# Optimization experiments

Hardware: AMD Instinct MI355X
Metric: run time of the kernel (lower is better)

The kernel has to match this reference:

```python
import jax, jax.numpy as jnp
import numpy as np

D_MODEL = 512
WINDOW = 128
N_HEADS = 8


def setup_inputs() -> dict:
    key = jax.random.key(0)
    k1, k2, k3, k4, k5 = jax.random.split(key, 5)
    B, S, D = 8, 4096, D_MODEL
    scale = 1.0 / np.sqrt(D)
    return {
        "x": jax.random.normal(k1, (B, S, D), dtype=jnp.float32),
        "in_proj_w": jax.random.normal(k2, (3 * D, D), dtype=jnp.float32) * scale,
        "in_proj_b": jax.random.normal(k3, (3 * D,), dtype=jnp.float32) * 0.02,
        "out_proj_w": jax.random.normal(k4, (D, D), dtype=jnp.float32) * scale,
        "out_proj_b": jax.random.normal(k5, (D,), dtype=jnp.float32) * 0.02,
    }


def reference(x, in_proj_w, in_proj_b, out_proj_w, out_proj_b):
    # Non-overlapping sliding-window MHA with shared weights per window.
    B, S, D = x.shape
    W = WINDOW
    H = N_HEADS
    hd = D // H
    nw = S // W  # S chosen divisible by window size

    xw = x.reshape(B, nw, W, D)
    # Fused QKV projection (torch in_proj_weight layout: [3D, D], y = x @ W^T + b)
    qkv = jnp.einsum("bnwd,ed->bnwe", xw, in_proj_w) + in_proj_b  # [B,nw,W,3D]
    q, k, v = jnp.split(qkv, 3, axis=-1)

    def to_heads(t):
        return t.reshape(B, nw, W, H, hd)

    q = to_heads(q) * (1.0 / np.sqrt(hd))
    k = to_heads(k)
    v = to_heads(v)

    # Block-diagonal attention: scores only within each window [B,nw,H,W,W]
    scores = jnp.einsum("bnqhd,bnkhd->bnhqk", q, k)
    attn = jax.nn.softmax(scores, axis=-1)
    ctx = jnp.einsum("bnhqk,bnkhd->bnqhd", attn, v)  # [B,nw,W,H,hd]
    ctx = ctx.reshape(B, S, D)

    out = jnp.einsum("bsd,ed->bse", ctx, out_proj_w) + out_proj_b
    return out
```

## Files before the change

### kernel.cpp

```cpp
#include <hip/hip_runtime.h>


typedef __bf16 bf16x8 __attribute__((ext_vector_type(8)));
typedef float  f32x4  __attribute__((ext_vector_type(4)));

#define MFMA16(a, b, c) __builtin_amdgcn_mfma_f32_16x16x32_bf16((a), (b), (c), 0, 0, 0)

#define VMCNT_(n) asm volatile("s_waitcnt vmcnt(" #n ")" ::: "memory")
#define VMCNT(n) VMCNT_(n)
#define LGKM0() asm volatile("s_waitcnt lgkmcnt(0)" ::: "memory")

__device__ __forceinline__ void gload_lds16(const __bf16* g, void* l) {
    __builtin_amdgcn_global_load_lds(
        (const __attribute__((address_space(1))) unsigned int*)g,
        (__attribute__((address_space(3))) unsigned int*)l, 16, 0, 0);
}

__device__ __forceinline__ void cvt8(const float* __restrict__ s,
                                     __bf16* __restrict__ d, long i) {
    const float4* s4 = reinterpret_cast<const float4*>(s);
    float4 a = s4[2 * i], b = s4[2 * i + 1];
    bf16x8 v;
    v[0] = (__bf16)a.x; v[1] = (__bf16)a.y; v[2] = (__bf16)a.z; v[3] = (__bf16)a.w;
    v[4] = (__bf16)b.x; v[5] = (__bf16)b.y; v[6] = (__bf16)b.z; v[7] = (__bf16)b.w;
    *reinterpret_cast<bf16x8*>(d + 8 * i) = v;
}

__global__ void convert_k(const float* __restrict__ x,
                          const float* __restrict__ w_in,
                          const float* __restrict__ w_out,
                          __bf16* __restrict__ x_bf,
                          __bf16* __restrict__ w_in_bf,
                          __bf16* __restrict__ w_out_bf)
{
    long i0 = (long)blockIdx.x * blockDim.x + threadIdx.x;
    long stride = (long)gridDim.x * blockDim.x;
    for (long i = i0; i < 16777216 / 8; i += stride) cvt8(x, x_bf, i);
    for (long i = i0; i < 786432 / 8;   i += stride) cvt8(w_in, w_in_bf, i);
    for (long i = i0; i < 262144 / 8;   i += stride) cvt8(w_out, w_out_bf, i);
}

template<int EPI, int NN>
__global__ __launch_bounds__(512, 2)
void gemm256(const __bf16* __restrict__ A,
             const __bf16* __restrict__ Bw,
             const float* __restrict__ bias,
             void* __restrict__ Cq,
             __bf16* __restrict__ vT)
{
    __shared__ __align__(16) char smem[131072];

    const int nwg = gridDim.x;
    const int chunk = nwg >> 3;
    const int bid = blockIdx.x;
    const int wg = (bid & 7) * chunk + (bid >> 3);
    const int nidx = wg % NN;
    const int midx = wg / NN;
    const long mbase = (long)midx * 256;
    const int colbase = nidx * 256;

    const int tid = threadIdx.x;
    const int w = tid >> 6, lane = tid & 63;
    const int lrow = lane & 15, hi = lane >> 4;
    const int quad = lane >> 4, sl = lane & 15;
    const int wm = w >> 2, wn = w & 3;

    const int l8 = lane >> 3;
    const int slotp = (lane & 7) ^ l8;
    const __bf16* stA = A  + (mbase + 8 * w + l8) * 512 + slotp * 8;
    const __bf16* stB = Bw + ((long)colbase + 8 * w + l8) * 512 + slotp * 8;
    const int ldsw = w * 1024;

    auto stage8 = [&](int tt) {
        char* As = smem + (tt & 1) * 32768;
        char* Bs = smem + 65536 + (tt & 1) * 32768;
        const int ko = tt * 64;
        gload_lds16(stA + ko,             As + ldsw);
        gload_lds16(stA + 64 * 512 + ko,  As + 8192 + ldsw);
        gload_lds16(stA + 128 * 512 + ko, As + 16384 + ldsw);
        gload_lds16(stA + 192 * 512 + ko, As + 24576 + ldsw);
        gload_lds16(stB + ko,             Bs + ldsw);
        gload_lds16(stB + 64 * 512 + ko,  Bs + 8192 + ldsw);
        gload_lds16(stB + 128 * 512 + ko, Bs + 16384 + ldsw);
        gload_lds16(stB + 192 * 512 + ko, Bs + 24576 + ldsw);
    };

    f32x4 acc[8][4];
    #pragma unroll
    for (int rt = 0; rt < 8; ++rt)
        #pragma unroll
        for (int ct = 0; ct < 4; ++ct) acc[rt][ct] = (f32x4){0.f, 0.f, 0.f, 0.f};

    bf16x8 af[4], bfr[4];

#define PHASE(T, KK, RT0, LB)                                                     \
    {                                                                             \
        const char* As = smem + ((T) & 1) * 32768;                                \
        const char* Bs = smem + 65536 + ((T) & 1) * 32768;                        \
        const int ko = ((KK) * 64 + hi * 16) ^ ((lrow & 7) << 4);                 \
        if (LB) {                                                                 \
            _Pragma("unroll")                                                     \
            for (int ct = 0; ct < 4; ++ct)                                        \
                bfr[ct] = *reinterpret_cast<const bf16x8*>(                       \
                    Bs + (64 * wn + 16 * ct + lrow) * 128 + ko);                  \
        }                                                                         \
        _Pragma("unroll")                                                         \
        for (int i = 0; i < 4; ++i)                                               \
            af[i] = *reinterpret_cast<const bf16x8*>(                             \
                As + (128 * wm + 16 * ((RT0) + i) + lrow) * 128 + ko);            \
        __builtin_amdgcn_s_setprio(1);                                            \
        _Pragma("unroll")                                                         \
        for (int i = 0; i < 4; ++i)                                               \
            _Pragma("unroll")                                                     \
            for (int ct = 0; ct < 4; ++ct)                                        \
                acc[(RT0) + i][ct] = MFMA16(af[i], bfr[ct], acc[(RT0) + i][ct]);  \
        __builtin_amdgcn_s_setprio(0);                                            \
    }

    stage8(0); stage8(1);
    VMCNT(8);
    __builtin_amdgcn_s_barrier();

    #pragma unroll 1
    for (int t = 0; t < 8; ++t) {
        if (t) {
            VMCNT(0);
            __builtin_amdgcn_s_barrier();
            if (t < 7) stage8(t + 1);
        }
        PHASE(t, 0, 0, 1);
        __builtin_amdgcn_s_barrier();
        PHASE(t, 0, 4, 0);
        __builtin_amdgcn_s_barrier();
        PHASE(t, 1, 0, 1);
        __builtin_amdgcn_s_barrier();
        PHASE(t, 1, 4, 0);
    }
#undef PHASE
    __builtin_amdgcn_s_barrier();

    const int colg0 = colbase + 64 * wn + lrow;
    if (EPI == 0) {
        if (colbase < 1024) {
            const float scale = (colbase < 512) ? 0.125f : 1.0f;
            __bf16* qk = (__bf16*)Cq;
            #pragma unroll
            for (int ct = 0; ct < 4; ++ct) {
                float b = bias[colg0 + 16 * ct];
                int col2 = (64 * wn + 16 * ct + lrow) * 2;
                #pragma unroll
                for (int rt = 0; rt < 8; ++rt)
                    #pragma unroll
                    for (int r = 0; r < 4; ++r) {
                        int row = 128 * wm + 16 * rt + 4 * hi + r;
                        *reinterpret_cast<__bf16*>(
                            smem + row * 512 + (col2 ^ ((row & 31) << 4))) =
                            (__bf16)((acc[rt][ct][r] + b) * scale);
                    }
            }
            LGKM0();
            __builtin_amdgcn_s_barrier();
            #pragma unroll
            for (int i = 0; i < 8; ++i) {
                int row = 32 * w + 4 * i + quad;
                #pragma unroll
                for (int h2 = 0; h2 < 2; ++h2) {
                    int slot = (16 * h2 + sl) ^ (row & 31);
                    bf16x8 v = *reinterpret_cast<const bf16x8*>(smem + row * 512 + slot * 16);
                    *reinterpret_cast<bf16x8*>(
                        qk + (mbase + row) * 1024 + colbase + h2 * 128 + sl * 8) = v;
                }
            }
        } else {
            #pragma unroll
            for (int ct = 0; ct < 4; ++ct) {
                float b = bias[colg0 + 16 * ct];
                int e = 64 * wn + 16 * ct + lrow;
                #pragma unroll
                for (int rt = 0; rt < 8; ++rt)
                    #pragma unroll
                    for (int r = 0; r < 4; ++r) {
                        int tok = 128 * wm + 16 * rt + 4 * hi + r;
                        *reinterpret_cast<__bf16*>(
                            smem + e * 512 + ((tok * 2) ^ ((e & 31) << 4))) =
                            (__bf16)(acc[rt][ct][r] + b);
                    }
            }
            LGKM0();
            __builtin_amdgcn_s_barrier();
            #pragma unroll
            for (int i = 0; i < 8; ++i) {
                int e = 32 * w + 4 * i + quad;
                #pragma unroll
                for (int h2 = 0; h2 < 2; ++h2) {
                    int slot = (16 * h2 + sl) ^ (e & 31);
                    bf16x8 v = *reinterpret_cast<const bf16x8*>(smem + e * 512 + slot * 16);
                    *reinterpret_cast<bf16x8*>(
                        vT + (long)(2 * midx + h2) * 65536 +
                        (colbase - 1024 + e) * 128 + sl * 8) = v;
                }
            }
        }
    } else {
        float* outp = (float*)Cq;
        float bb[4];
        #pragma unroll
        for (int ct = 0; ct < 4; ++ct) bb[ct] = bias[colg0 + 16 * ct];
        #pragma unroll 1
        for (int half = 0; half < 2; ++half) {
            if (wm == half) {
                #pragma unroll
                for (int ct = 0; ct < 4; ++ct) {
                    int c4 = (64 * wn + 16 * ct + lrow) * 4;
                    #pragma unroll
                    for (int rt = 0; rt < 8; ++rt)
                        #pragma unroll
                        for (int r = 0; r < 4; ++r) {
                            int row = 16 * rt + 4 * hi + r;
                            *reinterpret_cast<float*>(
                                smem + row * 1024 + (c4 ^ ((row & 63) << 4))) =
                                acc[rt][ct][r] + bb[ct];
                        }
                }
            }
            LGKM0();
            __builtin_amdgcn_s_barrier();
            #pragma unroll
            for (int i = 0; i < 4; ++i) {
                int row = 16 * w + 4 * i + quad;
                #pragma unroll
                for (int h2 = 0; h2 < 4; ++h2) {
                    int slot = (16 * h2 + sl) ^ (row & 63);
                    f32x4 v = *reinterpret_cast<const f32x4*>(smem + row * 1024 + slot * 16);
                    *reinterpret_cast<f32x4*>(
                        outp + (mbase + 128 * half + row) * 512 + colbase + h2 * 64 + sl * 4) = v;
                }
            }
            __builtin_amdgcn_s_barrier();
        }
    }
}

__global__ __launch_bounds__(256)
void swa_attn(const __bf16* __restrict__ qk,
              const __bf16* __restrict__ vT,
              __bf16* __restrict__ ctx)
{
    __shared__ __bf16 p_lds[4][32][136];

    const int bid = blockIdx.x;
    const int win = bid >> 3, h = bid & 7;
    const int tid = threadIdx.x;
    const int w = tid >> 6, lane = tid & 63;
    const int lrow = lane & 15, hi = lane >> 4;
    const long tokb = (long)win * 128;

    bf16x8 qa[2][2];
    #pragma unroll
    for (int rt = 0; rt < 2; ++rt)
        #pragma unroll
        for (int ks = 0; ks < 2; ++ks)
            qa[rt][ks] = *reinterpret_cast<const bf16x8*>(
                qk + (tokb + 32 * w + 16 * rt + lrow) * 1024 + h * 64 + ks * 32 + hi * 8);

    f32x4 s[2][8];
    #pragma unroll
    for (int rt = 0; rt < 2; ++rt)
        #pragma unroll
        for (int ct = 0; ct < 8; ++ct) s[rt][ct] = (f32x4){0.f, 0.f, 0.f, 0.f};
    #pragma unroll
    for (int ks = 0; ks < 2; ++ks) {
        #pragma unroll
        for (int ct = 0; ct < 8; ++ct) {
            bf16x8 kb = *reinterpret_cast<const bf16x8*>(
                qk + (tokb + 16 * ct + lrow) * 1024 + 512 + h * 64 + ks * 32 + hi * 8);
            s[0][ct] = MFMA16(qa[0][ks], kb, s[0][ct]);
            s[1][ct] = MFMA16(qa[1][ks], kb, s[1][ct]);
        }
    }

    float inv[2][4];
    #pragma unroll
    for (int rt = 0; rt < 2; ++rt) {
        #pragma unroll
        for (int r = 0; r < 4; ++r) {
            float m = s[rt][0][r];
            #pragma unroll
            for (int ct = 1; ct < 8; ++ct) m = fmaxf(m, s[rt][ct][r]);
            m = fmaxf(m, __shfl_xor(m, 1));
            m = fmaxf(m, __shfl_xor(m, 2));
            m = fmaxf(m, __shfl_xor(m, 4));
            m = fmaxf(m, __shfl_xor(m, 8));
            float sum = 0.f;
            #pragma unroll
            for (int ct = 0; ct < 8; ++ct) {
                float e = __expf(s[rt][ct][r] - m);
                sum += e;
                p_lds[w][16 * rt + 4 * hi + r][16 * ct + lrow] = (__bf16)e;
            }
            sum += __shfl_xor(sum, 1);
            sum += __shfl_xor(sum, 2);
            sum += __shfl_xor(sum, 4);
            sum += __shfl_xor(sum, 8);
            inv[rt][r] = 1.f / sum;
        }
    }

    f32x4 o[2][4];
    #pragma unroll
    for (int rt = 0; rt < 2; ++rt)
        #pragma unroll
        for (int ct = 0; ct < 4; ++ct) o[rt][ct] = (f32x4){0.f, 0.f, 0.f, 0.f};
    const __bf16* vb = vT + ((long)win * 8 + h) * 64 * 128;
    #pragma unroll
    for (int kt = 0; kt < 4; ++kt) {
        bf16x8 pa0 = *reinterpret_cast<const bf16x8*>(&p_lds[w][lrow][32 * kt + 8 * hi]);
        bf16x8 pa1 = *reinterpret_cast<const bf16x8*>(&p_lds[w][16 + lrow][32 * kt + 8 * hi]);
        #pragma unroll
        for (int ct = 0; ct < 4; ++ct) {
            bf16x8 vf = *reinterpret_cast<const bf16x8*>(
                vb + (16 * ct + lrow) * 128 + 32 * kt + 8 * hi);
            o[0][ct] = MFMA16(pa0, vf, o[0][ct]);
            o[1][ct] = MFMA16(pa1, vf, o[1][ct]);
        }
    }

    #pragma unroll
    for (int rt = 0; rt < 2; ++rt)
        #pragma unroll
        for (int ct = 0; ct < 4; ++ct)
            #pragma unroll
            for (int r = 0; r < 4; ++r) {
                long tok = tokb + 32 * w + 16 * rt + 4 * hi + r;
                ctx[tok * 512 + h * 64 + 16 * ct + lrow] =
                    (__bf16)(o[rt][ct][r] * inv[rt][r]);
            }
}

extern "C" void kernel_launch(void* const* d_in, const int* in_sizes, int n_in,
                              void* d_out, int out_size, void* d_ws, size_t ws_size,
                              hipStream_t stream)
{
    const float* x     = (const float*)d_in[0];
    const float* w_in  = (const float*)d_in[1];
    const float* b_in  = (const float*)d_in[2];
    const float* w_out = (const float*)d_in[3];
    const float* b_out = (const float*)d_in[4];

    char* ws = (char*)d_ws;
    __bf16* x_bf     = (__bf16*)(ws);
    __bf16* ctx      = (__bf16*)(ws);
    __bf16* vT       = (__bf16*)(ws + 33554432);
    __bf16* w_in_bf  = (__bf16*)(ws + 67108864);
    __bf16* w_out_bf = (__bf16*)(ws + 68681728);
    __bf16* qk       = (__bf16*)d_out;

    convert_k<<<2048, 256, 0, stream>>>(x, w_in, w_out, x_bf, w_in_bf, w_out_bf);
    gemm256<0, 6><<<768, 512, 0, stream>>>(x_bf, w_in_bf, b_in, (void*)qk, vT);
    swa_attn<<<2048, 256, 0, stream>>>(qk, vT, ctx);
    gemm256<1, 2><<<256, 512, 0, stream>>>(ctx, w_out_bf, b_out, d_out, nullptr);
}
```

Before: 177.2 us.

## Fuse QKV projection with windowed attention per window, simplify output GEMM epilogue

Replaces the separate QKV GEMM and attention kernels with one kernel where each block owns a 128-token window. It loops over heads, computes that head's Q/K/V slice of the projection into LDS, then does softmax attention in place. This avoids writing Q, K and V^T to global memory and reading them back. The cost is only 256 blocks, head-serial work with many barriers, and re-reading the x tile for every head. The output GEMM epilogue now writes scattered fp32 directly instead of staging through LDS for coalesced stores.

```diff
diff --git a/kernel.cpp b/kernel.cpp
--- a/kernel.cpp
+++ b/kernel.cpp
@@ -5,7 +5,6 @@
 typedef float  f32x4  __attribute__((ext_vector_type(4)));
 
 #define MFMA16(a, b, c) __builtin_amdgcn_mfma_f32_16x16x32_bf16((a), (b), (c), 0, 0, 0)
-
 #define VMCNT_(n) asm volatile("s_waitcnt vmcnt(" #n ")" ::: "memory")
 #define VMCNT(n) VMCNT_(n)
 #define LGKM0() asm volatile("s_waitcnt lgkmcnt(0)" ::: "memory")
@@ -40,13 +39,177 @@
     for (long i = i0; i < 262144 / 8;   i += stride) cvt8(w_out, w_out_bf, i);
 }
 
-template<int EPI, int NN>
 __global__ __launch_bounds__(512, 2)
-void gemm256(const __bf16* __restrict__ A,
-             const __bf16* __restrict__ Bw,
-             const float* __restrict__ bias,
-             void* __restrict__ Cq,
-             __bf16* __restrict__ vT)
+void swa_fused(const __bf16* __restrict__ x_bf,
+               const __bf16* __restrict__ w_in,
+               const float* __restrict__ b_in,
+               __bf16* __restrict__ ctx)
+{
+    __shared__ __align__(16) char smem[134144];
+    char* const ring = smem;
+    char* const q_l  = smem;
+    char* const k_l  = smem + 18432;
+    char* const vT_l = smem + 81920;
+    char* const p_l  = smem + 99328;
+
+    const int win = blockIdx.x;
+    const long tokb = (long)win * 128;
+    const int tid = threadIdx.x, w = tid >> 6, lane = tid & 63;
+    const int lrow = lane & 15, hi = lane >> 4;
+    const int rw = w >> 2, cw = w & 3;
+    const int l8 = lane >> 3;
+    const int slotp = (lane & 7) ^ l8;
+
+    const __bf16* Ax  = x_bf + (tokb + 8 * w + l8) * 512 + slotp * 8;
+    const __bf16* Bx0 = w_in + (long)(8 * w + l8) * 512 + slotp * 8;
+
+    auto stage = [&](int h, int t) {
+        char* buf = ring + (t & 1) * 40960;
+        const int ko = t * 64;
+        const __bf16* Bx = Bx0 + (long)h * 64 * 512;
+        gload_lds16(Ax + ko,                    buf + w * 1024);
+        gload_lds16(Ax + 64 * 512 + ko,         buf + 8192 + w * 1024);
+        gload_lds16(Bx + ko,                    buf + 16384 + w * 1024);
+        gload_lds16(Bx + (long)512 * 512 + ko,  buf + 24576 + w * 1024);
+        gload_lds16(Bx + (long)1024 * 512 + ko, buf + 32768 + w * 1024);
+    };
+
+    stage(0, 0);
+
+    #pragma unroll 1
+    for (int h = 0; h < 8; ++h) {
+        f32x4 acc[4][3];
+        #pragma unroll
+        for (int i = 0; i < 4; ++i)
+            #pragma unroll
+            for (int j = 0; j < 3; ++j) acc[i][j] = (f32x4){0.f, 0.f, 0.f, 0.f};
+
+        #pragma unroll 1
+        for (int t = 0; t < 8; ++t) {
+            VMCNT(0);
+            LGKM0();
+            __builtin_amdgcn_s_barrier();
+            if (t < 7) stage(h, t + 1);
+            const char* As = ring + (t & 1) * 40960;
+            const char* Bs = As + 16384;
+            #pragma unroll
+            for (int kk = 0; kk < 2; ++kk) {
+                const int ko = (kk * 64 + hi * 16) ^ ((lrow & 7) << 4);
+                bf16x8 af[4], bfr[3];
+                #pragma unroll
+                for (int i = 0; i < 4; ++i)
+                    af[i] = *reinterpret_cast<const bf16x8*>(
+                        As + (64 * rw + 16 * i + lrow) * 128 + ko);
+                #pragma unroll
+                for (int j = 0; j < 3; ++j)
+                    bfr[j] = *reinterpret_cast<const bf16x8*>(
+                        Bs + (48 * cw + 16 * j + lrow) * 128 + ko);
+                __builtin_amdgcn_s_setprio(1);
+                #pragma unroll
+                for (int i = 0; i < 4; ++i)
+                    #pragma unroll
+                    for (int j = 0; j < 3; ++j)
+                        acc[i][j] = MFMA16(af[i], bfr[j], acc[i][j]);
+                __builtin_amdgcn_s_setprio(0);
+            }
+        }
+        LGKM0();
+        __builtin_amdgcn_s_barrier();
+
+        #pragma unroll
+        for (int j = 0; j < 3; ++j) {
+            const int n = 48 * cw + 16 * j + lrow;
+            const int band = n >> 6, d = n & 63;
+            const float bb = b_in[band * 512 + h * 64 + d];
+            #pragma unroll
+            for (int i = 0; i < 4; ++i)
+                #pragma unroll
+                for (int r = 0; r < 4; ++r) {
+                    const int m = 64 * rw + 16 * i + 4 * hi + r;
+                    const float v = acc[i][j][r] + bb;
+                    if (band == 0)
+                        *reinterpret_cast<__bf16*>(q_l + m * 144 + d * 2) = (__bf16)(v * 0.125f);
+                    else if (band == 1)
+                        *reinterpret_cast<__bf16*>(k_l + m * 144 + d * 2) = (__bf16)v;
+                    else
+                        *reinterpret_cast<__bf16*>(vT_l + d * 272 + m * 2) = (__bf16)v;
+                }
+        }
+        LGKM0();
+        __builtin_amdgcn_s_barrier();
+
+        f32x4 s[8];
+        #pragma unroll
+        for (int ct = 0; ct < 8; ++ct) s[ct] = (f32x4){0.f, 0.f, 0.f, 0.f};
+        #pragma unroll
+        for (int kt = 0; kt < 2; ++kt) {
+            bf16x8 qa = *reinterpret_cast<const bf16x8*>(
+                q_l + (16 * w + lrow) * 144 + kt * 64 + hi * 16);
+            #pragma unroll
+            for (int ct = 0; ct < 8; ++ct) {
+                bf16x8 kb = *reinterpret_cast<const bf16x8*>(
+                    k_l + (16 * ct + lrow) * 144 + kt * 64 + hi * 16);
+                s[ct] = MFMA16(qa, kb, s[ct]);
+            }
+        }
+        LGKM0();
+        __builtin_amdgcn_s_barrier();
+        if (h < 7) stage(h + 1, 0);
+
+        float inv[4];
+        #pragma unroll
+        for (int r = 0; r < 4; ++r) {
+            float mx = s[0][r];
+            #pragma unroll
+            for (int ct = 1; ct < 8; ++ct) mx = fmaxf(mx, s[ct][r]);
+            mx = fmaxf(mx, __shfl_xor(mx, 1));
+            mx = fmaxf(mx, __shfl_xor(mx, 2));
+            mx = fmaxf(mx, __shfl_xor(mx, 4));
+            mx = fmaxf(mx, __shfl_xor(mx, 8));
+            float sum = 0.f;
+            #pragma unroll
+            for (int ct = 0; ct < 8; ++ct) {
+                float e = __expf(s[ct][r] - mx);
+                sum += e;
+                *reinterpret_cast<__bf16*>(
+                    p_l + w * 4352 + (4 * hi + r) * 272 + (16 * ct + lrow) * 2) = (__bf16)e;
+            }
+            sum += __shfl_xor(sum, 1);
+            sum += __shfl_xor(sum, 2);
+            sum += __shfl_xor(sum, 4);
+            sum += __shfl_xor(sum, 8);
+            inv[r] = 1.f / sum;
+        }
+
+        f32x4 o[4];
+        #pragma unroll
+        for (int ct = 0; ct < 4; ++ct) o[ct] = (f32x4){0.f, 0.f, 0.f, 0.f};
+        #pragma unroll
+        for (int kt = 0; kt < 4; ++kt) {
+            bf16x8 pa = *reinterpret_cast<const bf16x8*>(
+                p_l + w * 4352 + lrow * 272 + kt * 64 + hi * 16);
+            #pragma unroll
+            for (int ct = 0; ct < 4; ++ct) {
+                bf16x8 vf = *reinterpret_cast<const bf16x8*>(
+                    vT_l + (16 * ct + lrow) * 272 + kt * 64 + hi * 16);
+                o[ct] = MFMA16(pa, vf, o[ct]);
+            }
+        }
+        #pragma unroll
+        for (int ct = 0; ct < 4; ++ct)
+            #pragma unroll
+            for (int r = 0; r < 4; ++r) {
+                long tok = tokb + 16 * w + 4 * hi + r;
+                ctx[tok * 512 + h * 64 + 16 * ct + lrow] = (__bf16)(o[ct][r] * inv[r]);
+            }
+    }
+}
+
+__global__ __launch_bounds__(512, 2)
+void gemm_out(const __bf16* __restrict__ A,
+              const __bf16* __restrict__ Bw,
+              const float* __restrict__ bias,
+              float* __restrict__ out)
 {
     __shared__ __align__(16) char smem[131072];
 
@@ -54,15 +217,14 @@
     const int chunk = nwg >> 3;
     const int bid = blockIdx.x;
     const int wg = (bid & 7) * chunk + (bid >> 3);
-    const int nidx = wg % NN;
-    const int midx = wg / NN;
+    const int nidx = wg % 2;
+    const int midx = wg / 2;
     const long mbase = (long)midx * 256;
     const int colbase = nidx * 256;
 
     const int tid = threadIdx.x;
     const int w = tid >> 6, lane = tid & 63;
     const int lrow = lane & 15, hi = lane >> 4;
-    const int quad = lane >> 4, sl = lane & 15;
     const int wm = w >> 2, wn = w & 3;
 
     const int l8 = lane >> 3;
@@ -92,7 +254,6 @@
         for (int ct = 0; ct < 4; ++ct) acc[rt][ct] = (f32x4){0.f, 0.f, 0.f, 0.f};
 
     bf16x8 af[4], bfr[4];
-
 #define PHASE(T, KK, RT0, LB)                                                     \
     {                                                                             \
         const char* As = smem + ((T) & 1) * 32768;                                \
@@ -137,204 +298,19 @@
         PHASE(t, 1, 4, 0);
     }
 #undef PHASE
-    __builtin_amdgcn_s_barrier();
-
-    const int colg0 = colbase + 64 * wn + lrow;
-    if (EPI == 0) {
-        if (colbase < 1024) {
-            const float scale = (colbase < 512) ? 0.125f : 1.0f;
-            __bf16* qk = (__bf16*)Cq;
-            #pragma unroll
-            for (int ct = 0; ct < 4; ++ct) {
-                float b = bias[colg0 + 16 * ct];
-                int col2 = (64 * wn + 16 * ct + lrow) * 2;
-                #pragma unroll
-                for (int rt = 0; rt < 8; ++rt)
-                    #pragma unroll
-                    for (int r = 0; r < 4; ++r) {
-                        int row = 128 * wm + 16 * rt + 4 * hi + r;
-                        *reinterpret_cast<__bf16*>(
-                            smem + row * 512 + (col2 ^ ((row & 31) << 4))) =
-                            (__bf16)((acc[rt][ct][r] + b) * scale);
-                    }
-            }
-            LGKM0();
-            __builtin_amdgcn_s_barrier();
-            #pragma unroll
-            for (int i = 0; i < 8; ++i) {
-                int row = 32 * w + 4 * i + quad;
-                #pragma unroll
-                for (int h2 = 0; h2 < 2; ++h2) {
-                    int slot = (16 * h2 + sl) ^ (row & 31);
-                    bf16x8 v = *reinterpret_cast<const bf16x8*>(smem + row * 512 + slot * 16);
-                    *reinterpret_cast<bf16x8*>(
-                        qk + (mbase + row) * 1024 + colbase + h2 * 128 + sl * 8) = v;
-                }
-            }
-        } else {
-            #pragma unroll
-            for (int ct = 0; ct < 4; ++ct) {
-                float b = bias[colg0 + 16 * ct];
-                int e = 64 * wn + 16 * ct + lrow;
-                #pragma unroll
-                for (int rt = 0; rt < 8; ++rt)
-                    #pragma unroll
-                    for (int r = 0; r < 4; ++r) {
-                        int tok = 128 * wm + 16 * rt + 4 * hi + r;
-                        *reinterpret_cast<__bf16*>(
-                            smem + e * 512 + ((tok * 2) ^ ((e & 31) << 4))) =
-                            (__bf16)(acc[rt][ct][r] + b);
-                    }
-            }
-            LGKM0();
-            __builtin_amdgcn_s_barrier();
-            #pragma unroll
-            for (int i = 0; i < 8; ++i) {
-                int e = 32 * w + 4 * i + quad;
-                #pragma unroll
-                for (int h2 = 0; h2 < 2; ++h2) {
-                    int slot = (16 * h2 + sl) ^ (e & 31);
-                    bf16x8 v = *reinterpret_cast<const bf16x8*>(smem + e * 512 + slot * 16);
-                    *reinterpret_cast<bf16x8*>(
-                        vT + (long)(2 * midx + h2) * 65536 +
-                        (colbase - 1024 + e) * 128 + sl * 8) = v;
-                }
-            }
-        }
-    } else {
-        float* outp = (float*)Cq;
-        float bb[4];
-        #pragma unroll
-        for (int ct = 0; ct < 4; ++ct) bb[ct] = bias[colg0 + 16 * ct];
-        #pragma unroll 1
-        for (int half = 0; half < 2; ++half) {
-            if (wm == half) {
-                #pragma unroll
-                for (int ct = 0; ct < 4; ++ct) {
-                    int c4 = (64 * wn + 16 * ct + lrow) * 4;
-                    #pragma unroll
-                    for (int rt = 0; rt < 8; ++rt)
-                        #pragma unroll
-                        for (int r = 0; r < 4; ++r) {
-                            int row = 16 * rt + 4 * hi + r;
-                            *reinterpret_cast<float*>(
-                                smem + row * 1024 + (c4 ^ ((row & 63) << 4))) =
-                                acc[rt][ct][r] + bb[ct];
-                        }
-                }
-            }
-            LGKM0();
-            __builtin_amdgcn_s_barrier();
-            #pragma unroll
-            for (int i = 0; i < 4; ++i) {
-                int row = 16 * w + 4 * i + quad;
-                #pragma unroll
-                for (int h2 = 0; h2 < 4; ++h2) {
-                    int slot = (16 * h2 + sl) ^ (row & 63);
-                    f32x4 v = *reinterpret_cast<const f32x4*>(smem + row * 1024 + slot * 16);
-                    *reinterpret_cast<f32x4*>(
-                        outp + (mbase + 128 * half + row) * 512 + colbase + h2 * 64 + sl * 4) = v;
-                }
-            }
-            __builtin_amdgcn_s_barrier();
+
+    #pragma unroll
+    for (int ct = 0; ct < 4; ++ct) {
+        int colg = colbase + 64 * wn + 16 * ct + lrow;
+        float b = bias[colg];
+        #pragma unroll
+        for (int rt = 0; rt < 8; ++rt) {
+            long row = mbase + 128 * wm + 16 * rt + 4 * hi;
+            #pragma unroll
+            for (int r = 0; r < 4; ++r)
+                out[(row + r) * 512 + colg] = acc[rt][ct][r] + b;
         }
     }
-}
-
-__global__ __launch_bounds__(256)
-void swa_attn(const __bf16* __restrict__ qk,
-              const __bf16* __restrict__ vT,
-              __bf16* __restrict__ ctx)
-{
-    __shared__ __bf16 p_lds[4][32][136];
-
-    const int bid = blockIdx.x;
-    const int win = bid >> 3, h = bid & 7;
-    const int tid = threadIdx.x;
-    const int w = tid >> 6, lane = tid & 63;
-    const int lrow = lane & 15, hi = lane >> 4;
-    const long tokb = (long)win * 128;
-
-    bf16x8 qa[2][2];
-    #pragma unroll
-    for (int rt = 0; rt < 2; ++rt)
-        #pragma unroll
-        for (int ks = 0; ks < 2; ++ks)
-            qa[rt][ks] = *reinterpret_cast<const bf16x8*>(
-                qk + (tokb + 32 * w + 16 * rt + lrow) * 1024 + h * 64 + ks * 32 + hi * 8);
-
-    f32x4 s[2][8];
-    #pragma unroll
-    for (int rt = 0; rt < 2; ++rt)
-        #pragma unroll
-        for (int ct = 0; ct < 8; ++ct) s[rt][ct] = (f32x4){0.f, 0.f, 0.f, 0.f};
-    #pragma unroll
-    for (int ks = 0; ks < 2; ++ks) {
-        #pragma unroll
-        for (int ct = 0; ct < 8; ++ct) {
-            bf16x8 kb = *reinterpret_cast<const bf16x8*>(
-                qk + (tokb + 16 * ct + lrow) * 1024 + 512 + h * 64 + ks * 32 + hi * 8);
-            s[0][ct] = MFMA16(qa[0][ks], kb, s[0][ct]);
-            s[1][ct] = MFMA16(qa[1][ks], kb, s[1][ct]);
-        }
-    }
-
-    float inv[2][4];
-    #pragma unroll
-    for (int rt = 0; rt < 2; ++rt) {
-        #pragma unroll
-        for (int r = 0; r < 4; ++r) {
-            float m = s[rt][0][r];
-            #pragma unroll
-            for (int ct = 1; ct < 8; ++ct) m = fmaxf(m, s[rt][ct][r]);
-            m = fmaxf(m, __shfl_xor(m, 1));
-            m = fmaxf(m, __shfl_xor(m, 2));
-            m = fmaxf(m, __shfl_xor(m, 4));
-            m = fmaxf(m, __shfl_xor(m, 8));
-            float sum = 0.f;
-            #pragma unroll
-            for (int ct = 0; ct < 8; ++ct) {
-                float e = __expf(s[rt][ct][r] - m);
-                sum += e;
-                p_lds[w][16 * rt + 4 * hi + r][16 * ct + lrow] = (__bf16)e;
-            }
-            sum += __shfl_xor(sum, 1);
-            sum += __shfl_xor(sum, 2);
-            sum += __shfl_xor(sum, 4);
-            sum += __shfl_xor(sum, 8);
-            inv[rt][r] = 1.f / sum;
-        }
-    }
-
-    f32x4 o[2][4];
-    #pragma unroll
-    for (int rt = 0; rt < 2; ++rt)
-        #pragma unroll
-        for (int ct = 0; ct < 4; ++ct) o[rt][ct] = (f32x4){0.f, 0.f, 0.f, 0.f};
-    const __bf16* vb = vT + ((long)win * 8 + h) * 64 * 128;
-    #pragma unroll
-    for (int kt = 0; kt < 4; ++kt) {
-        bf16x8 pa0 = *reinterpret_cast<const bf16x8*>(&p_lds[w][lrow][32 * kt + 8 * hi]);
-        bf16x8 pa1 = *reinterpret_cast<const bf16x8*>(&p_lds[w][16 + lrow][32 * kt + 8 * hi]);
-        #pragma unroll
-        for (int ct = 0; ct < 4; ++ct) {
-            bf16x8 vf = *reinterpret_cast<const bf16x8*>(
-                vb + (16 * ct + lrow) * 128 + 32 * kt + 8 * hi);
-            o[0][ct] = MFMA16(pa0, vf, o[0][ct]);
-            o[1][ct] = MFMA16(pa1, vf, o[1][ct]);
-        }
-    }
-
-    #pragma unroll
-    for (int rt = 0; rt < 2; ++rt)
-        #pragma unroll
-        for (int ct = 0; ct < 4; ++ct)
-            #pragma unroll
-            for (int r = 0; r < 4; ++r) {
-                long tok = tokb + 32 * w + 16 * rt + 4 * hi + r;
-                ctx[tok * 512 + h * 64 + 16 * ct + lrow] =
-                    (__bf16)(o[rt][ct][r] * inv[rt][r]);
-            }
 }
 
 extern "C" void kernel_launch(void* const* d_in, const int* in_sizes, int n_in,
@@ -349,14 +325,11 @@
 
     char* ws = (char*)d_ws;
     __bf16* x_bf     = (__bf16*)(ws);
-    __bf16* ctx      = (__bf16*)(ws);
-    __bf16* vT       = (__bf16*)(ws + 33554432);
+    __bf16* ctx      = (__bf16*)(ws + 33554432);
     __bf16* w_in_bf  = (__bf16*)(ws + 67108864);
     __bf16* w_out_bf = (__bf16*)(ws + 68681728);
-    __bf16* qk       = (__bf16*)d_out;
 
     convert_k<<<2048, 256, 0, stream>>>(x, w_in, w_out, x_bf, w_in_bf, w_out_bf);
-    gemm256<0, 6><<<768, 512, 0, stream>>>(x_bf, w_in_bf, b_in, (void*)qk, vT);
-    swa_attn<<<2048, 256, 0, stream>>>(qk, vT, ctx);
-    gemm256<1, 2><<<256, 512, 0, stream>>>(ctx, w_out_bf, b_out, d_out, nullptr);
-}
+    swa_fused<<<256, 512, 0, stream>>>(x_bf, w_in_bf, b_in, ctx);
+    gemm_out<<<256, 512, 0, stream>>>(ctx, w_out_bf, b_out, (float*)d_out);
+}
```

Result: faster. 154.7 us (-12.7%).

## Split GEMM K-tiles into half stages with finer-grained prefetch and direct output stores

Applied to the files above, without the earlier changes.

Restructures the GEMM main loop so each 64-wide K step is staged as two 32-wide halves for A and B separately. Each global-to-LDS load is issued between MFMA phases with partial vmcnt waits, which replaces the full drain and barrier at the top of every iteration. The LDS layout changes to 64-byte rows with a new XOR swizzle. Separately, the fp32 output epilogue drops the LDS transpose and writes scalar floats straight to global memory, which removes barriers but gives uncoalesced stores.

```diff
diff --git a/kernel.cpp b/kernel.cpp
--- a/kernel.cpp
+++ b/kernel.cpp
@@ -5,7 +5,6 @@
 typedef float  f32x4  __attribute__((ext_vector_type(4)));
 
 #define MFMA16(a, b, c) __builtin_amdgcn_mfma_f32_16x16x32_bf16((a), (b), (c), 0, 0, 0)
-
 #define VMCNT_(n) asm volatile("s_waitcnt vmcnt(" #n ")" ::: "memory")
 #define VMCNT(n) VMCNT_(n)
 #define LGKM0() asm volatile("s_waitcnt lgkmcnt(0)" ::: "memory")
@@ -65,25 +64,12 @@
     const int quad = lane >> 4, sl = lane & 15;
     const int wm = w >> 2, wn = w & 3;
 
-    const int l8 = lane >> 3;
-    const int slotp = (lane & 7) ^ l8;
-    const __bf16* stA = A  + (mbase + 8 * w + l8) * 512 + slotp * 8;
-    const __bf16* stB = Bw + ((long)colbase + 8 * w + l8) * 512 + slotp * 8;
-    const int ldsw = w * 1024;
-
-    auto stage8 = [&](int tt) {
-        char* As = smem + (tt & 1) * 32768;
-        char* Bs = smem + 65536 + (tt & 1) * 32768;
-        const int ko = tt * 64;
-        gload_lds16(stA + ko,             As + ldsw);
-        gload_lds16(stA + 64 * 512 + ko,  As + 8192 + ldsw);
-        gload_lds16(stA + 128 * 512 + ko, As + 16384 + ldsw);
-        gload_lds16(stA + 192 * 512 + ko, As + 24576 + ldsw);
-        gload_lds16(stB + ko,             Bs + ldsw);
-        gload_lds16(stB + 64 * 512 + ko,  Bs + 8192 + ldsw);
-        gload_lds16(stB + 128 * 512 + ko, Bs + 16384 + ldsw);
-        gload_lds16(stB + 192 * 512 + ko, Bs + 24576 + ldsw);
-    };
+    const int srow = tid >> 2;
+    const int kchunk = (tid & 3) ^ ((srow >> 1) & 3);
+    const __bf16* PA = A  + (mbase + srow) * 512 + kchunk * 8;
+    const __bf16* PB = Bw + ((long)colbase + srow) * 512 + kchunk * 8;
+    const int sbase = w * 1024;
+    const int rd16 = (hi ^ ((lrow >> 1) & 3)) << 4;
 
     f32x4 acc[8][4];
     #pragma unroll
@@ -91,53 +77,67 @@
         #pragma unroll
         for (int ct = 0; ct < 4; ++ct) acc[rt][ct] = (f32x4){0.f, 0.f, 0.f, 0.f};
 
+#define STG(TT, ISB, KK) {                                                        \
+        char* d_ = smem + (ISB) * 65536 + ((TT) & 1) * 32768 + (KK) * 16384 + sbase; \
+        const __bf16* p_ = ((ISB) ? PB : PA) + (TT) * 64 + (KK) * 32;             \
+        gload_lds16(p_, d_);                                                      \
+        gload_lds16(p_ + 128 * 512, d_ + 8192); }
+
     bf16x8 af[4], bfr[4];
-
-#define PHASE(T, KK, RT0, LB)                                                     \
-    {                                                                             \
-        const char* As = smem + ((T) & 1) * 32768;                                \
-        const char* Bs = smem + 65536 + ((T) & 1) * 32768;                        \
-        const int ko = ((KK) * 64 + hi * 16) ^ ((lrow & 7) << 4);                 \
-        if (LB) {                                                                 \
-            _Pragma("unroll")                                                     \
-            for (int ct = 0; ct < 4; ++ct)                                        \
-                bfr[ct] = *reinterpret_cast<const bf16x8*>(                       \
-                    Bs + (64 * wn + 16 * ct + lrow) * 128 + ko);                  \
-        }                                                                         \
+#define RDB(T, KK) {                                                              \
+        const char* Bb_ = smem + 65536 + ((T) & 1) * 32768 + (KK) * 16384;        \
+        _Pragma("unroll")                                                         \
+        for (int ct = 0; ct < 4; ++ct)                                            \
+            bfr[ct] = *reinterpret_cast<const bf16x8*>(                           \
+                Bb_ + (64 * wn + 16 * ct + lrow) * 64 + rd16); }
+#define RDA(T, KK, R0) {                                                          \
+        const char* Ab_ = smem + ((T) & 1) * 32768 + (KK) * 16384;                \
         _Pragma("unroll")                                                         \
         for (int i = 0; i < 4; ++i)                                               \
             af[i] = *reinterpret_cast<const bf16x8*>(                             \
-                As + (128 * wm + 16 * ((RT0) + i) + lrow) * 128 + ko);            \
+                Ab_ + (128 * wm + 16 * ((R0) + i) + lrow) * 64 + rd16); }
+#define FMA(R0) {                                                                 \
         __builtin_amdgcn_s_setprio(1);                                            \
         _Pragma("unroll")                                                         \
         for (int i = 0; i < 4; ++i)                                               \
             _Pragma("unroll")                                                     \
             for (int ct = 0; ct < 4; ++ct)                                        \
-                acc[(RT0) + i][ct] = MFMA16(af[i], bfr[ct], acc[(RT0) + i][ct]);  \
-        __builtin_amdgcn_s_setprio(0);                                            \
-    }
-
-    stage8(0); stage8(1);
-    VMCNT(8);
+                acc[(R0) + i][ct] = MFMA16(af[i], bfr[ct], acc[(R0) + i][ct]);    \
+        __builtin_amdgcn_s_setprio(0); }
+
+    STG(0, 0, 0); STG(0, 1, 0); STG(0, 0, 1); STG(0, 1, 1);
+    VMCNT(4);
     __builtin_amdgcn_s_barrier();
 
     #pragma unroll 1
     for (int t = 0; t < 8; ++t) {
-        if (t) {
-            VMCNT(0);
-            __builtin_amdgcn_s_barrier();
-            if (t < 7) stage8(t + 1);
-        }
-        PHASE(t, 0, 0, 1);
+        if (t < 7) STG(t + 1, 0, 0);
+        RDB(t, 0); RDA(t, 0, 0);
+        LGKM0();
         __builtin_amdgcn_s_barrier();
-        PHASE(t, 0, 4, 0);
+        FMA(0);
+        if (t < 7) STG(t + 1, 1, 0);
+        RDA(t, 0, 4);
+        if (t < 7) { VMCNT(4); } else { VMCNT(0); }
+        LGKM0();
         __builtin_amdgcn_s_barrier();
-        PHASE(t, 1, 0, 1);
+        FMA(4);
+        if (t < 7) STG(t + 1, 0, 1);
+        RDB(t, 1); RDA(t, 1, 0);
+        LGKM0();
         __builtin_amdgcn_s_barrier();
-        PHASE(t, 1, 4, 0);
-    }
-#undef PHASE
-    __builtin_amdgcn_s_barrier();
+        FMA(0);
+        if (t < 7) STG(t + 1, 1, 1);
+        RDA(t, 1, 4);
+        if (t < 7) { VMCNT(4); } else { VMCNT(0); }
+        LGKM0();
+        __builtin_amdgcn_s_barrier();
+        FMA(4);
+    }
+#undef STG
+#undef RDB
+#undef RDA
+#undef FMA
 
     const int colg0 = colbase + 64 * wn + lrow;
     if (EPI == 0) {
@@ -203,40 +203,17 @@
         }
     } else {
         float* outp = (float*)Cq;
-        float bb[4];
-        #pragma unroll
-        for (int ct = 0; ct < 4; ++ct) bb[ct] = bias[colg0 + 16 * ct];
-        #pragma unroll 1
-        for (int half = 0; half < 2; ++half) {
-            if (wm == half) {
-                #pragma unroll
-                for (int ct = 0; ct < 4; ++ct) {
-                    int c4 = (64 * wn + 16 * ct + lrow) * 4;
-                    #pragma unroll
-                    for (int rt = 0; rt < 8; ++rt)
-                        #pragma unroll
-                        for (int r = 0; r < 4; ++r) {
-                            int row = 16 * rt + 4 * hi + r;
-                            *reinterpret_cast<float*>(
-                                smem + row * 1024 + (c4 ^ ((row & 63) << 4))) =
-                                acc[rt][ct][r] + bb[ct];
-                        }
-                }
-            }
-            LGKM0();
-            __builtin_amdgcn_s_barrier();
-            #pragma unroll
-            for (int i = 0; i < 4; ++i) {
-                int row = 16 * w + 4 * i + quad;
-                #pragma unroll
-                for (int h2 = 0; h2 < 4; ++h2) {
-                    int slot = (16 * h2 + sl) ^ (row & 63);
-                    f32x4 v = *reinterpret_cast<const f32x4*>(smem + row * 1024 + slot * 16);
-                    *reinterpret_cast<f32x4*>(
-                        outp + (mbase + 128 * half + row) * 512 + colbase + h2 * 64 + sl * 4) = v;
-                }
-            }
-            __builtin_amdgcn_s_barrier();
+        #pragma unroll
+        for (int ct = 0; ct < 4; ++ct) {
+            int colg = colbase + 64 * wn + 16 * ct + lrow;
+            float b = bias[colg];
+            #pragma unroll
+            for (int rt = 0; rt < 8; ++rt) {
+                long row = mbase + 128 * wm + 16 * rt + 4 * hi;
+                #pragma unroll
+                for (int r = 0; r < 4; ++r)
+                    outp[(row + r) * 512 + colg] = acc[rt][ct][r] + b;
+            }
         }
     }
 }
```

Result: faster. 165.3 us (-6.7%).
